# Kernel tuning notes

Measured on AMD Instinct MI355X. Metric: run time of the kernel, lower is better.

The kernel has to match this reference:

```python
import jax, jax.numpy as jnp
import numpy as np

BS, SL, FD = 8192, 49, 11
D_MODEL, DM2, HEAD = 128, 64, 8
NH, NHID, NLAYER = DM2 // HEAD, 4, 2
ABF = 1.0
XY_IDX = np.array([0, 1, 2, 3, 4, 5, 6, 7, 10])  # x feats + y feat (batch-normed cols)
DEC_IN = D_MODEL + 10  # d_model + len(x_dims + spa_dims)


def tanhshrink(x):
    return x - jnp.tanh(x)


def rope_angles(spa):
    # spa: [bs, sl, 2] -> per-token block angles [bs, sl, 4]
    # block order matches torch.block_diag(Rx(t0), Ry(t0), Rx(t1), Ry(t1))
    thetas = 10000.0 ** ((2.0 - 2.0 * jnp.arange(2, dtype=spa.dtype)) / 8.0)  # d=8, n_thetas=2
    ax = spa[..., 0:1] * thetas  # [bs, sl, 2]
    ay = spa[..., 1:2] * thetas
    return jnp.stack([ax[..., 0], ay[..., 0], ax[..., 1], ay[..., 1]], axis=-1)


def apply_rope(v, ang):
    # v: [bs, nh, s, 8]; ang: [bs, s, 4]. Applies the 8x8 block-diagonal
    # rotation directly on 2-d sub-pairs (same math as R @ v, no 8x8 matmats).
    c = jnp.cos(ang)[:, None]  # [bs, 1, s, 4]
    s = jnp.sin(ang)[:, None]
    v2 = v.reshape(*v.shape[:-1], 4, 2)
    r = jnp.stack([c * v2[..., 0] - s * v2[..., 1],
                   s * v2[..., 0] + c * v2[..., 1]], axis=-1)
    return r.reshape(v.shape)


def heads(x):  # [bs, s, dm2] -> [bs, nh, s, hd]
    b, s, _ = x.shape
    return x.reshape(b, s, NH, HEAD).transpose(0, 2, 1, 3)


def merge(x):  # [bs, nh, s, hd] -> [bs, s, dm2]
    b, h, s, d = x.shape
    return x.transpose(0, 2, 1, 3).reshape(b, s, h * d)


def mlp2(x, w1, b1, w2, b2):
    return tanhshrink(x @ w1 + b1) @ w2 + b2


def forward_impl(input_tensor, dists, bn_gamma, bn_beta,
                 xe_w1, xe_b1, xe_w2, xe_b2, ye_w1, ye_b1, ye_w2, ye_b2,
                 learnable_y, hidden_tokens, Wq, Wk, Wv, Wo, Wq2, Wk2, Wv2, Wo2,
                 dec_w0, dec_b0, dec_w1, dec_b1, dec_w2, dec_b2):
    bs = input_tensor.shape[0]
    # --- NanBatchNorm over x+y feature columns (no NaNs in clean inputs) ---
    xy = input_tensor[:, :, XY_IDX]
    mu = jnp.mean(xy, axis=(0, 1), keepdims=True)
    var = jnp.var(xy, axis=(0, 1), keepdims=True)
    xy = (xy - mu) / jnp.sqrt(var + 1e-5) * bn_gamma + bn_beta
    input_tensor = input_tensor.at[:, :, XY_IDX].set(xy)

    # --- target at last seq position: drop its dist, keep context dists ---
    dists_ctx = dists[:, :-1]                       # [bs, sl-1]
    central_x = input_tensor[:, -1:, :-1]           # [bs, 1, 10] (x + spa feats)

    # --- 2D RoPE angles from spatial coords ---
    ang = rope_angles(input_tensor[:, :, 8:10])     # [bs, sl, 4]

    # --- FCN encoders (two streams a=x, b=y) ---
    x_embed = mlp2(input_tensor[:, :, :8], xe_w1, xe_b1, xe_w2, xe_b2)      # [bs, sl, 64]
    y_embed = mlp2(input_tensor[:, :-1, 10:11], ye_w1, ye_b1, ye_w2, ye_b2)  # [bs, sl-1, 64]
    y_embed = jnp.concatenate([y_embed, jnp.broadcast_to(learnable_y, (bs, 1, DM2))], axis=1)

    ctx = (x_embed[:, :-1], y_embed[:, :-1])
    qry = (x_embed[:, -1:], y_embed[:, -1:])
    ang_ctx, ang_q = ang[:, :-1], ang[:, -1:]
    bias = (-ABF * dists_ctx)[:, None, None, :]     # [bs, 1, 1, sl-1]
    scale = 1.0 / jnp.sqrt(jnp.asarray(HEAD, input_tensor.dtype))

    outs, attn_ws = [], []
    for s in range(2):
        H = jnp.broadcast_to(hidden_tokens, (bs, NHID, DM2))
        for l in range(NLAYER):
            q = heads(H @ Wq[l, s])
            k = apply_rope(heads(ctx[s] @ Wk[l, s]), ang_ctx)
            v = heads(ctx[s] @ Wv[l, s])
            sc = jnp.einsum('bhqd,bhkd->bhqk', q, k) * scale + bias
            a = jax.nn.softmax(sc, axis=-1)
            H = H + merge(jnp.einsum('bhqk,bhkd->bhqd', a, v)) @ Wo[l, s]
        # query cross-attends the inducing tokens
        q = apply_rope(heads(qry[s] @ Wq2[s]), ang_q)
        k = heads(H @ Wk2[s])
        v = heads(H @ Wv2[s])
        sc = jnp.einsum('bhqd,bhkd->bhqk', q, k) * scale
        a = jax.nn.softmax(sc, axis=-1)
        outs.append(merge(jnp.einsum('bhqk,bhkd->bhqd', a, v)) @ Wo2[s])  # [bs, 1, 64]
        attn_ws.append(a)

    encoding = jnp.concatenate(outs, axis=-1)               # [bs, 1, 128]
    encoding = jnp.concatenate([encoding, central_x], axis=-1)  # [bs, 1, 138]
    h = tanhshrink(encoding @ dec_w0 + dec_b0)
    h = tanhshrink(h @ dec_w1 + dec_b1)
    pred = h @ dec_w2 + dec_b2                              # [bs, 1, 1]
    return pred


def setup_inputs() -> dict:
    key = jax.random.key(0)
    ks = jax.random.split(key, 32)
    g = lambda i, shape: 0.05 * jax.random.normal(ks[i], shape, dtype=jnp.float32)
    inp = {
        'input_tensor': jax.random.normal(ks[0], (BS, SL, FD), dtype=jnp.float32),
        'dists': jax.random.uniform(ks[1], (BS, SL), dtype=jnp.float32),
        'target_position': jnp.zeros((3, BS), dtype=jnp.int32),
        'bn_gamma': jnp.ones((9,), jnp.float32),
        'bn_beta': jnp.zeros((9,), jnp.float32),
        'xe_w1': g(2, (8, DM2)), 'xe_b1': jnp.zeros((DM2,), jnp.float32),
        'xe_w2': g(3, (DM2, DM2)), 'xe_b2': jnp.zeros((DM2,), jnp.float32),
        'ye_w1': g(4, (1, DM2)), 'ye_b1': jnp.zeros((DM2,), jnp.float32),
        'ye_w2': g(5, (DM2, DM2)), 'ye_b2': jnp.zeros((DM2,), jnp.float32),
        'learnable_y': g(6, (1, 1, DM2)),
        'hidden_tokens': g(7, (NHID, DM2)),
        'Wq': g(8, (NLAYER, 2, DM2, DM2)), 'Wk': g(9, (NLAYER, 2, DM2, DM2)),
        'Wv': g(10, (NLAYER, 2, DM2, DM2)), 'Wo': g(11, (NLAYER, 2, DM2, DM2)),
        'Wq2': g(12, (2, DM2, DM2)), 'Wk2': g(13, (2, DM2, DM2)),
        'Wv2': g(14, (2, DM2, DM2)), 'Wo2': g(15, (2, DM2, DM2)),
        'dec_w0': g(16, (DEC_IN, 512)), 'dec_b0': jnp.zeros((512,), jnp.float32),
        'dec_w1': g(17, (512, 256)), 'dec_b1': jnp.zeros((256,), jnp.float32),
        'dec_w2': g(18, (256, 1)), 'dec_b2': jnp.zeros((1,), jnp.float32),
    }
    return inp


def reference(input_tensor, dists, target_position, bn_gamma, bn_beta,
              xe_w1, xe_b1, xe_w2, xe_b2, ye_w1, ye_b1, ye_w2, ye_b2,
              learnable_y, hidden_tokens, Wq, Wk, Wv, Wo, Wq2, Wk2, Wv2, Wo2,
              dec_w0, dec_b0, dec_w1, dec_b1, dec_w2, dec_b2):
    # target_position is an index constant (query is the last token by construction)
    return forward_impl(input_tensor, dists, bn_gamma, bn_beta,
                        xe_w1, xe_b1, xe_w2, xe_b2, ye_w1, ye_b1, ye_w2, ye_b2,
                        learnable_y, hidden_tokens, Wq, Wk, Wv, Wo, Wq2, Wk2, Wv2, Wo2,
                        dec_w0, dec_b0, dec_w1, dec_b1, dec_w2, dec_b2)
```

## Files before the change

### kernel.cpp

```cpp
#include <hip/hip_runtime.h>
#include <math.h>

#define BS 8192
#define SL 49
#define FDIM 11
#define ROWS (BS*SL)

__device__ __forceinline__ float tanhshrink_f(float x) {
  float e = __expf(2.f * x);
  return (x - 1.f) + __fdividef(2.f, e + 1.f);
}

__global__ __launch_bounds__(256) void k_stats(const float* __restrict__ inp,
                                               double* __restrict__ gsum) {
  const int nblk = gridDim.x;
  const int per = (ROWS + nblk - 1) / nblk;
  const int r0 = blockIdx.x * per;
  int r1 = r0 + per; if (r1 > ROWS) r1 = ROWS;
  float s[9], q[9];
#pragma unroll
  for (int j = 0; j < 9; ++j) { s[j] = 0.f; q[j] = 0.f; }
  for (int r = r0 + threadIdx.x; r < r1; r += 256) {
    const float* row = inp + r * FDIM;
#pragma unroll
    for (int j = 0; j < 9; ++j) {
      float v = row[j < 8 ? j : 10];
      s[j] += v; q[j] += v * v;
    }
  }
#pragma unroll
  for (int j = 0; j < 9; ++j) {
    for (int off = 32; off; off >>= 1) {
      s[j] += __shfl_down(s[j], off);
      q[j] += __shfl_down(q[j], off);
    }
  }
  __shared__ float red[4][18];
  const int wid = threadIdx.x >> 6;
  const int lane = threadIdx.x & 63;
  if (lane == 0) {
#pragma unroll
    for (int j = 0; j < 9; ++j) { red[wid][j] = s[j]; red[wid][9 + j] = q[j]; }
  }
  __syncthreads();
  if (threadIdx.x < 18) {
    float t = red[0][threadIdx.x] + red[1][threadIdx.x] +
              red[2][threadIdx.x] + red[3][threadIdx.x];
    atomicAdd(&gsum[threadIdx.x], (double)t);
  }
}

__global__ __launch_bounds__(256) void k_finalize(const double* __restrict__ gsum,
                           const float* __restrict__ gamma,
                           const float* __restrict__ beta,
                           const float* __restrict__ hidden,
                           const float* __restrict__ Wq,
                           float* __restrict__ bnp,
                           float* __restrict__ q0g) {
  int tid = threadIdx.x;
  if (tid < 9) {
    const double N = (double)ROWS;
    double mean = gsum[tid] / N;
    double msq  = gsum[9 + tid] / N;
    float var = (float)(msq - mean * mean);
    float sc = gamma[tid] / sqrtf(var + 1e-5f);
    bnp[tid] = sc;
    bnp[9 + tid] = beta[tid] - (float)mean * sc;
  }
  int s = tid >> 7, i2 = (tid >> 6) & 1, c = tid & 63;
  const float* W = Wq + (s << 12);
#pragma unroll
  for (int ii = 0; ii < 2; ++ii) {
    int i = i2 + 2 * ii;
    float a = 0.f;
    for (int k = 0; k < 64; ++k) a += hidden[i * 64 + k] * W[k * 64 + c];
    q0g[s * 256 + i * 64 + c] = a;
  }
}

__global__ __launch_bounds__(256, 4) void k_mega(
    const float* __restrict__ inp, const float* __restrict__ dists,
    const float* __restrict__ bnp, const float* __restrict__ q0g,
    const float* __restrict__ xe_w1, const float* __restrict__ xe_b1,
    const float* __restrict__ xe_w2, const float* __restrict__ xe_b2,
    const float* __restrict__ ye_w1, const float* __restrict__ ye_b1,
    const float* __restrict__ ye_w2, const float* __restrict__ ye_b2,
    const float* __restrict__ learnable_y, const float* __restrict__ hidden_tokens,
    const float* __restrict__ Wq, const float* __restrict__ Wk,
    const float* __restrict__ Wv, const float* __restrict__ Wo,
    const float* __restrict__ Wq2, const float* __restrict__ Wk2,
    const float* __restrict__ Wv2, const float* __restrict__ Wo2,
    float* __restrict__ enc)
{
  __shared__ float raw[49][12];
  __shared__ float cs8[49][8];
  __shared__ float emb[49][64];
  __shared__ float KB[49][68];
  __shared__ float scb[32][52];
  __shared__ float Hs[4][64];
  __shared__ float qb[4][64];
  __shared__ float db[48];
  __shared__ float bnl[18];
  __shared__ float q2[64];
  __shared__ float o1[64];
  __shared__ float a2[32];

  const int tid  = threadIdx.x;
  const int lane = tid & 63;
  const int grp  = tid >> 6;
  const int b    = blockIdx.x >> 1;
  const int s    = blockIdx.x & 1;
  const float scale = 0.35355339059327373f;

  for (int i = tid; i < 49 * FDIM; i += 256) raw[i / FDIM][i % FDIM] = inp[b * (49*FDIM) + i];
  if (tid < 18) bnl[tid] = bnp[tid];
  if (tid >= 64 && tid < 112) db[tid - 64] = dists[b * 49 + (tid - 64)];
  __syncthreads();

  if (tid < 49) {
    float x = raw[tid][8], y = raw[tid][9];
    cs8[tid][0] = cosf(10.f * x); cs8[tid][1] = cosf(10.f * y);
    cs8[tid][2] = cosf(x);        cs8[tid][3] = cosf(y);
    cs8[tid][4] = sinf(10.f * x); cs8[tid][5] = sinf(10.f * y);
    cs8[tid][6] = sinf(x);        cs8[tid][7] = sinf(y);
  }
  for (int i = tid; i < 441; i += 256) {
    int t = i / 9, j = i - t * 9;
    int f = (j < 8) ? j : 10;
    raw[t][f] = raw[t][f] * bnl[j] + bnl[9 + j];
  }
  __syncthreads();

  if (s == 0 && tid < 10) enc[b * 138 + 128 + tid] = raw[48][tid];

  if (s == 0) {
    const float bias1 = xe_b1[lane];
    float acc[13];
#pragma unroll
    for (int j = 0; j < 13; ++j) acc[j] = bias1;
#pragma unroll
    for (int k = 0; k < 8; ++k) {
      float w = xe_w1[k * 64 + lane];
#pragma unroll
      for (int j = 0; j < 13; ++j) {
        int t = grp + 4 * j;
        if (t < 49) acc[j] += raw[t][k] * w;
      }
    }
#pragma unroll
    for (int j = 0; j < 13; ++j) {
      int t = grp + 4 * j;
      if (t < 49) KB[t][lane] = tanhshrink_f(acc[j]);
    }
  } else {
    const float w1y = ye_w1[lane];
    const float b1y = ye_b1[lane];
#pragma unroll
    for (int j = 0; j < 12; ++j) {
      int t = grp + 4 * j;
      KB[t][lane] = tanhshrink_f(raw[t][10] * w1y + b1y);
    }
  }
  __syncthreads();

  if (s == 0) {
    const float b2 = xe_b2[lane];
    float acc[13];
#pragma unroll
    for (int j = 0; j < 13; ++j) acc[j] = b2;
    for (int k = 0; k < 64; k += 4) {
      float w0 = xe_w2[(k + 0) * 64 + lane];
      float w1_ = xe_w2[(k + 1) * 64 + lane];
      float w2_ = xe_w2[(k + 2) * 64 + lane];
      float w3_ = xe_w2[(k + 3) * 64 + lane];
#pragma unroll
      for (int j = 0; j < 13; ++j) {
        int t = grp + 4 * j;
        if (t < 49) {
          float4 cv = *(const float4*)&KB[t][k];
          acc[j] += cv.x * w0 + cv.y * w1_ + cv.z * w2_ + cv.w * w3_;
        }
      }
    }
#pragma unroll
    for (int j = 0; j < 13; ++j) {
      int t = grp + 4 * j;
      if (t < 49) emb[t][lane] = acc[j];
    }
  } else {
    const float b2 = ye_b2[lane];
    float acc[12];
#pragma unroll
    for (int j = 0; j < 12; ++j) acc[j] = b2;
    for (int k = 0; k < 64; k += 4) {
      float w0 = ye_w2[(k + 0) * 64 + lane];
      float w1_ = ye_w2[(k + 1) * 64 + lane];
      float w2_ = ye_w2[(k + 2) * 64 + lane];
      float w3_ = ye_w2[(k + 3) * 64 + lane];
#pragma unroll
      for (int j = 0; j < 12; ++j) {
        float4 cv = *(const float4*)&KB[grp + 4 * j][k];
        acc[j] += cv.x * w0 + cv.y * w1_ + cv.z * w2_ + cv.w * w3_;
      }
    }
#pragma unroll
    for (int j = 0; j < 12; ++j) emb[grp + 4 * j][lane] = acc[j];
    if (tid < 64) emb[48][lane] = learnable_y[lane];
  }
  Hs[grp][lane] = hidden_tokens[grp * 64 + lane];
  __syncthreads();

#pragma unroll 1
  for (int l = 0; l < 2; ++l) {
    const float* Wk_p = Wk + ((l * 2 + s) << 12);
    const float* Wv_p = Wv + ((l * 2 + s) << 12);
    const float* Wo_p = Wo + ((l * 2 + s) << 12);
    if (l == 0) {
      qb[grp][lane] = q0g[s * 256 + tid];
    } else {
      const float* Wq_p = Wq + ((l * 2 + s) << 12);
      float a = 0.f;
      for (int k = 0; k < 64; k += 4) {
        float4 hv = *(const float4*)&Hs[grp][k];
        a += hv.x * Wq_p[(k + 0) * 64 + lane] + hv.y * Wq_p[(k + 1) * 64 + lane]
           + hv.z * Wq_p[(k + 2) * 64 + lane] + hv.w * Wq_p[(k + 3) * 64 + lane];
      }
      qb[grp][lane] = a;
    }
    {
      float aK[12];
#pragma unroll
      for (int j = 0; j < 12; ++j) aK[j] = 0.f;
      for (int k = 0; k < 64; k += 4) {
        float wk0 = Wk_p[(k + 0) * 64 + lane], wk1 = Wk_p[(k + 1) * 64 + lane];
        float wk2 = Wk_p[(k + 2) * 64 + lane], wk3 = Wk_p[(k + 3) * 64 + lane];
#pragma unroll
        for (int j = 0; j < 12; ++j) {
          float4 cv = *(const float4*)&emb[grp + 4 * j][k];
          aK[j] += cv.x * wk0 + cv.y * wk1 + cv.z * wk2 + cv.w * wk3;
        }
      }
      const int p = (lane >> 1) & 3;
      const int odd = lane & 1;
#pragma unroll
      for (int j = 0; j < 12; ++j) {
        int t = grp + 4 * j;
        float other = __shfl_xor(aK[j], 1);
        float co = cs8[t][p], si = cs8[t][4 + p];
        KB[t][lane] = odd ? (si * other + co * aK[j]) : (co * aK[j] - si * other);
      }
    }
    __syncthreads();
    {
      const int t0 = tid & 7;
      const int i  = (tid >> 3) & 3;
      const int h  = tid >> 5;
      const int r  = tid >> 3;
      float4 qa = *(const float4*)&qb[i][h * 8];
      float4 qc = *(const float4*)&qb[i][h * 8 + 4];
      float v[6];
#pragma unroll
      for (int j = 0; j < 6; ++j) {
        int t = t0 + 8 * j;
        float4 ka = *(const float4*)&KB[t][h * 8];
        float4 kc = *(const float4*)&KB[t][h * 8 + 4];
        float a = qa.x * ka.x + qa.y * ka.y + qa.z * ka.z + qa.w * ka.w
                + qc.x * kc.x + qc.y * kc.y + qc.z * kc.z + qc.w * kc.w;
        v[j] = a * scale - db[t];
      }
      float m = fmaxf(fmaxf(fmaxf(v[0], v[1]), fmaxf(v[2], v[3])), fmaxf(v[4], v[5]));
      m = fmaxf(m, __shfl_xor(m, 1));
      m = fmaxf(m, __shfl_xor(m, 2));
      m = fmaxf(m, __shfl_xor(m, 4));
      float sum = 0.f;
#pragma unroll
      for (int j = 0; j < 6; ++j) { v[j] = __expf(v[j] - m); sum += v[j]; }
      sum += __shfl_xor(sum, 1);
      sum += __shfl_xor(sum, 2);
      sum += __shfl_xor(sum, 4);
      float inv = 1.f / sum;
#pragma unroll
      for (int j = 0; j < 6; ++j) scb[r][t0 + 8 * j] = v[j] * inv;
    }
    __syncthreads();
    {
      float acc[8];
#pragma unroll
      for (int m = 0; m < 8; ++m) acc[m] = 0.f;
      for (int tt = 0; tt < 48; tt += 4) {
        float e0 = emb[tt + 0][lane], e1 = emb[tt + 1][lane];
        float e2 = emb[tt + 2][lane], e3 = emb[tt + 3][lane];
#pragma unroll
        for (int m = 0; m < 8; ++m) {
          float4 sc4 = *(const float4*)&scb[grp + 4 * m][tt];
          acc[m] += sc4.x * e0 + sc4.y * e1 + sc4.z * e2 + sc4.w * e3;
        }
      }
#pragma unroll
      for (int m = 0; m < 8; ++m) KB[grp + 4 * m][lane] = acc[m];
    }
    __syncthreads();
    {
      const int r = ((lane >> 3) << 2) + grp;
      float a = 0.f;
      for (int c = 0; c < 64; c += 4) {
        float4 tv = *(const float4*)&KB[r][c];
        a += tv.x * Wv_p[(c + 0) * 64 + lane] + tv.y * Wv_p[(c + 1) * 64 + lane]
           + tv.z * Wv_p[(c + 2) * 64 + lane] + tv.w * Wv_p[(c + 3) * 64 + lane];
      }
      qb[grp][lane] = a;
    }
    __syncthreads();
    {
      float a = Hs[grp][lane];
      for (int k = 0; k < 64; k += 4) {
        float4 av = *(const float4*)&qb[grp][k];
        a += av.x * Wo_p[(k + 0) * 64 + lane] + av.y * Wo_p[(k + 1) * 64 + lane]
           + av.z * Wo_p[(k + 2) * 64 + lane] + av.w * Wo_p[(k + 3) * 64 + lane];
      }
      Hs[grp][lane] = a;
    }
    __syncthreads();
  }

  const float* Wq2_p = Wq2 + (s << 12);
  const float* Wk2_p = Wk2 + (s << 12);
  const float* Wv2_p = Wv2 + (s << 12);
  const float* Wo2_p = Wo2 + (s << 12);
  if (tid < 64) {
    float a = 0.f;
    for (int k = 0; k < 64; k += 4) {
      float4 cv = *(const float4*)&emb[48][k];
      a += cv.x * Wq2_p[(k + 0) * 64 + lane] + cv.y * Wq2_p[(k + 1) * 64 + lane]
         + cv.z * Wq2_p[(k + 2) * 64 + lane] + cv.w * Wq2_p[(k + 3) * 64 + lane];
    }
    float other = __shfl_xor(a, 1);
    int p = (lane >> 1) & 3;
    float co = cs8[48][p], si = cs8[48][4 + p];
    q2[lane] = (lane & 1) ? (si * other + co * a) : (co * a - si * other);
  }
  {
    float aK = 0.f, aV = 0.f;
    for (int k = 0; k < 64; k += 4) {
      float4 hv = *(const float4*)&Hs[grp][k];
      aK += hv.x * Wk2_p[(k + 0) * 64 + lane] + hv.y * Wk2_p[(k + 1) * 64 + lane]
          + hv.z * Wk2_p[(k + 2) * 64 + lane] + hv.w * Wk2_p[(k + 3) * 64 + lane];
      aV += hv.x * Wv2_p[(k + 0) * 64 + lane] + hv.y * Wv2_p[(k + 1) * 64 + lane]
          + hv.z * Wv2_p[(k + 2) * 64 + lane] + hv.w * Wv2_p[(k + 3) * 64 + lane];
    }
    KB[grp][lane] = aK;
    KB[8 + grp][lane] = aV;
  }
  __syncthreads();
  if (tid < 32) {
    int h = tid >> 2, i = tid & 3;
    float a = 0.f;
#pragma unroll
    for (int d = 0; d < 8; ++d) a += q2[h * 8 + d] * KB[i][h * 8 + d];
    a *= scale;
    float m = fmaxf(a, __shfl_xor(a, 1));
    m = fmaxf(m, __shfl_xor(m, 2));
    float e = __expf(a - m);
    float sum = e + __shfl_xor(e, 1);
    sum += __shfl_xor(sum, 2);
    a2[tid] = e / sum;
  }
  __syncthreads();
  if (tid < 64) {
    int h = lane >> 3;
    float a = 0.f;
#pragma unroll
    for (int i = 0; i < 4; ++i) a += a2[h * 4 + i] * KB[8 + i][lane];
    o1[lane] = a;
  }
  __syncthreads();
  if (tid < 64) {
    float a = 0.f;
    for (int k = 0; k < 64; k += 4) {
      float4 ov = *(const float4*)&o1[k];
      a += ov.x * Wo2_p[(k + 0) * 64 + lane] + ov.y * Wo2_p[(k + 1) * 64 + lane]
         + ov.z * Wo2_p[(k + 2) * 64 + lane] + ov.w * Wo2_p[(k + 3) * 64 + lane];
    }
    enc[b * 138 + s * 64 + lane] = a;
  }
}

__global__ __launch_bounds__(256) void k_dec(
    const float* __restrict__ enc,
    const float* __restrict__ w0, const float* __restrict__ b0,
    const float* __restrict__ w1, const float* __restrict__ b1,
    const float* __restrict__ w2, const float* __restrict__ b2,
    float* __restrict__ out)
{
  __shared__ float encs[16][140];
  __shared__ float h0s[16][512];
  __shared__ float h1s[16][256];
  const int tid = threadIdx.x;
  const int rb = blockIdx.x * 16;

  for (int i = tid; i < 16 * 138; i += 256) {
    int r = i / 138, k = i - r * 138;
    encs[r][k] = enc[(rb + r) * 138 + k];
  }
  __syncthreads();
  {
    float acc0[16], acc1[16];
    const float bb0 = b0[tid], bb1 = b0[tid + 256];
#pragma unroll
    for (int r = 0; r < 16; ++r) { acc0[r] = bb0; acc1[r] = bb1; }
    for (int k = 0; k < 136; k += 4) {
      float wa0 = w0[(k + 0) * 512 + tid], wa1 = w0[(k + 1) * 512 + tid];
      float wa2 = w0[(k + 2) * 512 + tid], wa3 = w0[(k + 3) * 512 + tid];
      float wb0 = w0[(k + 0) * 512 + tid + 256], wb1 = w0[(k + 1) * 512 + tid + 256];
      float wb2 = w0[(k + 2) * 512 + tid + 256], wb3 = w0[(k + 3) * 512 + tid + 256];
#pragma unroll
      for (int r = 0; r < 16; ++r) {
        float4 ev = *(const float4*)&encs[r][k];
        acc0[r] += ev.x * wa0 + ev.y * wa1 + ev.z * wa2 + ev.w * wa3;
        acc1[r] += ev.x * wb0 + ev.y * wb1 + ev.z * wb2 + ev.w * wb3;
      }
    }
    for (int k = 136; k < 138; ++k) {
      float wa = w0[k * 512 + tid], wb = w0[k * 512 + tid + 256];
#pragma unroll
      for (int r = 0; r < 16; ++r) {
        float e = encs[r][k];
        acc0[r] += e * wa; acc1[r] += e * wb;
      }
    }
#pragma unroll
    for (int r = 0; r < 16; ++r) {
      float a = acc0[r]; h0s[r][tid] = a - tanhf(a);
      a = acc1[r];       h0s[r][tid + 256] = a - tanhf(a);
    }
  }
  __syncthreads();
  {
    float acc[16];
    const float bb = b1[tid];
#pragma unroll
    for (int r = 0; r < 16; ++r) acc[r] = bb;
    for (int k = 0; k < 512; k += 4) {
      float ww0 = w1[(k + 0) * 256 + tid], ww1 = w1[(k + 1) * 256 + tid];
      float ww2 = w1[(k + 2) * 256 + tid], ww3 = w1[(k + 3) * 256 + tid];
#pragma unroll
      for (int r = 0; r < 16; ++r) {
        float4 hv = *(const float4*)&h0s[r][k];
        acc[r] += hv.x * ww0 + hv.y * ww1 + hv.z * ww2 + hv.w * ww3;
      }
    }
#pragma unroll
    for (int r = 0; r < 16; ++r) { float a = acc[r]; h1s[r][tid] = a - tanhf(a); }
  }
  __syncthreads();
  {
    int r = tid >> 4, l16 = tid & 15;
    float a = 0.f;
    for (int kk = 0; kk < 16; ++kk) {
      int k = l16 + 16 * kk;
      a += h1s[r][k] * w2[k];
    }
    for (int off = 8; off; off >>= 1) a += __shfl_down(a, off, 16);
    if (l16 == 0) out[rb + r] = a + b2[0];
  }
}

extern "C" void kernel_launch(void* const* d_in, const int* in_sizes, int n_in,
                              void* d_out, int out_size, void* d_ws, size_t ws_size,
                              hipStream_t stream) {
  const float* inp        = (const float*)d_in[0];
  const float* dists      = (const float*)d_in[1];
  const float* bn_gamma   = (const float*)d_in[3];
  const float* bn_beta    = (const float*)d_in[4];
  const float* xe_w1      = (const float*)d_in[5];
  const float* xe_b1      = (const float*)d_in[6];
  const float* xe_w2      = (const float*)d_in[7];
  const float* xe_b2      = (const float*)d_in[8];
  const float* ye_w1      = (const float*)d_in[9];
  const float* ye_b1      = (const float*)d_in[10];
  const float* ye_w2      = (const float*)d_in[11];
  const float* ye_b2      = (const float*)d_in[12];
  const float* learnable  = (const float*)d_in[13];
  const float* hidden     = (const float*)d_in[14];
  const float* Wq         = (const float*)d_in[15];
  const float* Wk         = (const float*)d_in[16];
  const float* Wv         = (const float*)d_in[17];
  const float* Wo         = (const float*)d_in[18];
  const float* Wq2        = (const float*)d_in[19];
  const float* Wk2        = (const float*)d_in[20];
  const float* Wv2        = (const float*)d_in[21];
  const float* Wo2        = (const float*)d_in[22];
  const float* dec_w0     = (const float*)d_in[23];
  const float* dec_b0     = (const float*)d_in[24];
  const float* dec_w1     = (const float*)d_in[25];
  const float* dec_b1     = (const float*)d_in[26];
  const float* dec_w2     = (const float*)d_in[27];
  const float* dec_b2     = (const float*)d_in[28];

  double* gsum = (double*)d_ws;
  float*  bnp  = (float*)((char*)d_ws + 256);
  float*  q0g  = (float*)((char*)d_ws + 512);
  float*  enc  = (float*)((char*)d_ws + 2560);

  hipMemsetAsync(d_ws, 0, 256, stream);
  k_stats   <<<512, 256, 0, stream>>>(inp, gsum);
  k_finalize<<<1, 256, 0, stream>>>(gsum, bn_gamma, bn_beta, hidden, Wq, bnp, q0g);
  k_mega    <<<BS * 2, 256, 0, stream>>>(inp, dists, bnp, q0g,
                                         xe_w1, xe_b1, xe_w2, xe_b2,
                                         ye_w1, ye_b1, ye_w2, ye_b2,
                                         learnable, hidden,
                                         Wq, Wk, Wv, Wo, Wq2, Wk2, Wv2, Wo2, enc);
  k_dec     <<<BS / 16, 256, 0, stream>>>(enc, dec_w0, dec_b0, dec_w1, dec_b1,
                                          dec_w2, dec_b2, (float*)d_out);
}
```

Measured before the change: 1.009 ms.

## Use split-bf16 MFMA for embedding second layer and K projections

Replaces the FP32 FMA loops for the encoder second MLP layer and the per-layer K projections with 16x16x32 bf16 MFMA instructions. Both operands are split into high and low bf16 halves (three MFMAs per step), which keeps close to fp32 accuracy. A new prep kernel pre-splits and transposes the weights each call. Shared memory is repacked with aliased buffers and XOR-swizzled bf16 tiles, the last token's embedding is computed separately, and launch bounds drop to 3 waves per SIMD. It trades extra MFMA work and conversion overhead for fewer VALU cycles, at some risk of small precision drift.

```diff
diff --git a/kernel.cpp b/kernel.cpp
--- a/kernel.cpp
+++ b/kernel.cpp
@@ -6,6 +6,17 @@
 #define FDIM 11
 #define ROWS (BS*SL)
 
+typedef __attribute__((ext_vector_type(8))) short bf16x8;
+typedef __attribute__((ext_vector_type(4))) float f32x4;
+
+__device__ __forceinline__ unsigned short f2bf(float f) {
+  unsigned u = __float_as_uint(f);
+  u += 0x7FFFu + ((u >> 16) & 1u);
+  return (unsigned short)(u >> 16);
+}
+__device__ __forceinline__ float bf2f(unsigned short h) {
+  return __uint_as_float(((unsigned)h) << 16);
+}
 __device__ __forceinline__ float tanhshrink_f(float x) {
   float e = __expf(2.f * x);
   return (x - 1.f) + __fdividef(2.f, e + 1.f);
@@ -78,47 +89,76 @@
   }
 }
 
-__global__ __launch_bounds__(256, 4) void k_mega(
+__global__ __launch_bounds__(256) void k_prep(const float* __restrict__ xe_w2,
+                                              const float* __restrict__ ye_w2,
+                                              const float* __restrict__ Wk,
+                                              unsigned short* __restrict__ wb) {
+  int idx = blockIdx.x * 256 + threadIdx.x;
+  int mat = idx >> 12;
+  int e = idx & 4095;
+  int n = e >> 6, k = e & 63;
+  float v; unsigned short *dh, *dl;
+  if (mat == 0)      { v = xe_w2[k * 64 + n]; dh = wb;          dl = wb + 4096;  }
+  else if (mat == 1) { v = ye_w2[k * 64 + n]; dh = wb + 8192;   dl = wb + 12288; }
+  else { int m = mat - 2; v = Wk[(m << 12) + k * 64 + n];
+         dh = wb + 16384 + (m << 12); dl = wb + 32768 + (m << 12); }
+  unsigned short h = f2bf(v);
+  dh[e] = h;
+  dl[e] = f2bf(v - bf2f(h));
+}
+
+__global__ __launch_bounds__(256, 3) void k_mega(
     const float* __restrict__ inp, const float* __restrict__ dists,
     const float* __restrict__ bnp, const float* __restrict__ q0g,
+    const unsigned short* __restrict__ wb,
     const float* __restrict__ xe_w1, const float* __restrict__ xe_b1,
     const float* __restrict__ xe_w2, const float* __restrict__ xe_b2,
     const float* __restrict__ ye_w1, const float* __restrict__ ye_b1,
-    const float* __restrict__ ye_w2, const float* __restrict__ ye_b2,
+    const float* __restrict__ ye_b2,
     const float* __restrict__ learnable_y, const float* __restrict__ hidden_tokens,
-    const float* __restrict__ Wq, const float* __restrict__ Wk,
+    const float* __restrict__ Wq,
     const float* __restrict__ Wv, const float* __restrict__ Wo,
     const float* __restrict__ Wq2, const float* __restrict__ Wk2,
     const float* __restrict__ Wv2, const float* __restrict__ Wo2,
     float* __restrict__ enc)
 {
-  __shared__ float raw[49][12];
-  __shared__ float cs8[49][8];
-  __shared__ float emb[49][64];
-  __shared__ float KB[49][68];
-  __shared__ float scb[32][52];
-  __shared__ float Hs[4][64];
-  __shared__ float qb[4][64];
-  __shared__ float db[48];
-  __shared__ float bnl[18];
-  __shared__ float q2[64];
-  __shared__ float o1[64];
-  __shared__ float a2[32];
+  __shared__ __align__(16) float KBf[48 * 68];
+  __shared__ __align__(16) unsigned short AstBuf[2 * 48 * 72];
+  __shared__ __align__(16) float embf[48 * 64];
+  __shared__ __align__(16) unsigned short EMBh[48 * 64];
+  __shared__ __align__(16) unsigned short EMBl[48 * 64];
+  __shared__ __align__(16) float cs8[49][8];
+  __shared__ __align__(16) float Hs[4 * 64];
+
+  float* rawp = KBf;
+  float* h1q  = KBf + 588;
+  float* bnlp = KBf + 652;
+  unsigned short* Asth = AstBuf;
+  unsigned short* Astl = AstBuf + 48 * 72;
+  float* fbuf = (float*)AstBuf;
+  float* scb  = fbuf;
+  float* qbf  = fbuf + 1664;
+  float* dbp  = fbuf + 1920;
+  float* embq = fbuf + 1968;
+  float* q2   = fbuf + 2032;
+  float* o1   = fbuf + 2096;
+  float* a2   = fbuf + 2160;
 
   const int tid  = threadIdx.x;
   const int lane = tid & 63;
   const int grp  = tid >> 6;
+  const int l15  = lane & 15;
+  const int quad = lane >> 4;
   const int b    = blockIdx.x >> 1;
   const int s    = blockIdx.x & 1;
   const float scale = 0.35355339059327373f;
 
-  for (int i = tid; i < 49 * FDIM; i += 256) raw[i / FDIM][i % FDIM] = inp[b * (49*FDIM) + i];
-  if (tid < 18) bnl[tid] = bnp[tid];
-  if (tid >= 64 && tid < 112) db[tid - 64] = dists[b * 49 + (tid - 64)];
+  for (int i = tid; i < 49 * FDIM; i += 256) rawp[(i / FDIM) * 12 + (i % FDIM)] = inp[b * (49 * FDIM) + i];
+  if (tid < 18) bnlp[tid] = bnp[tid];
   __syncthreads();
 
   if (tid < 49) {
-    float x = raw[tid][8], y = raw[tid][9];
+    float x = rawp[tid * 12 + 8], y = rawp[tid * 12 + 9];
     cs8[tid][0] = cosf(10.f * x); cs8[tid][1] = cosf(10.f * y);
     cs8[tid][2] = cosf(x);        cs8[tid][3] = cosf(y);
     cs8[tid][4] = sinf(10.f * x); cs8[tid][5] = sinf(10.f * y);
@@ -127,127 +167,144 @@
   for (int i = tid; i < 441; i += 256) {
     int t = i / 9, j = i - t * 9;
     int f = (j < 8) ? j : 10;
-    raw[t][f] = raw[t][f] * bnl[j] + bnl[9 + j];
-  }
-  __syncthreads();
-
-  if (s == 0 && tid < 10) enc[b * 138 + 128 + tid] = raw[48][tid];
+    rawp[t * 12 + f] = rawp[t * 12 + f] * bnlp[j] + bnlp[9 + j];
+  }
+  __syncthreads();
+
+  if (s == 0 && tid < 10) enc[b * 138 + 128 + tid] = rawp[48 * 12 + tid];
 
   if (s == 0) {
     const float bias1 = xe_b1[lane];
-    float acc[13];
-#pragma unroll
-    for (int j = 0; j < 13; ++j) acc[j] = bias1;
+    float acc[12];
+    float acc12 = bias1;
+#pragma unroll
+    for (int j = 0; j < 12; ++j) acc[j] = bias1;
 #pragma unroll
     for (int k = 0; k < 8; ++k) {
       float w = xe_w1[k * 64 + lane];
 #pragma unroll
-      for (int j = 0; j < 13; ++j) {
-        int t = grp + 4 * j;
-        if (t < 49) acc[j] += raw[t][k] * w;
-      }
-    }
-#pragma unroll
-    for (int j = 0; j < 13; ++j) {
+      for (int j = 0; j < 12; ++j) acc[j] += rawp[(grp + 4 * j) * 12 + k] * w;
+      acc12 += rawp[48 * 12 + k] * w;
+    }
+#pragma unroll
+    for (int j = 0; j < 12; ++j) {
       int t = grp + 4 * j;
-      if (t < 49) KB[t][lane] = tanhshrink_f(acc[j]);
-    }
+      float a = tanhshrink_f(acc[j]);
+      unsigned short h = f2bf(a);
+      Asth[t * 72 + lane] = h;
+      Astl[t * 72 + lane] = f2bf(a - bf2f(h));
+    }
+    if (grp == 0) h1q[lane] = tanhshrink_f(acc12);
   } else {
     const float w1y = ye_w1[lane];
     const float b1y = ye_b1[lane];
 #pragma unroll
     for (int j = 0; j < 12; ++j) {
       int t = grp + 4 * j;
-      KB[t][lane] = tanhshrink_f(raw[t][10] * w1y + b1y);
-    }
-  }
-  __syncthreads();
-
-  if (s == 0) {
-    const float b2 = xe_b2[lane];
-    float acc[13];
-#pragma unroll
-    for (int j = 0; j < 13; ++j) acc[j] = b2;
-    for (int k = 0; k < 64; k += 4) {
-      float w0 = xe_w2[(k + 0) * 64 + lane];
-      float w1_ = xe_w2[(k + 1) * 64 + lane];
-      float w2_ = xe_w2[(k + 2) * 64 + lane];
-      float w3_ = xe_w2[(k + 3) * 64 + lane];
-#pragma unroll
-      for (int j = 0; j < 13; ++j) {
-        int t = grp + 4 * j;
-        if (t < 49) {
-          float4 cv = *(const float4*)&KB[t][k];
-          acc[j] += cv.x * w0 + cv.y * w1_ + cv.z * w2_ + cv.w * w3_;
-        }
-      }
-    }
-#pragma unroll
-    for (int j = 0; j < 13; ++j) {
-      int t = grp + 4 * j;
-      if (t < 49) emb[t][lane] = acc[j];
-    }
-  } else {
-    const float b2 = ye_b2[lane];
-    float acc[12];
-#pragma unroll
-    for (int j = 0; j < 12; ++j) acc[j] = b2;
-    for (int k = 0; k < 64; k += 4) {
-      float w0 = ye_w2[(k + 0) * 64 + lane];
-      float w1_ = ye_w2[(k + 1) * 64 + lane];
-      float w2_ = ye_w2[(k + 2) * 64 + lane];
-      float w3_ = ye_w2[(k + 3) * 64 + lane];
-#pragma unroll
-      for (int j = 0; j < 12; ++j) {
-        float4 cv = *(const float4*)&KB[grp + 4 * j][k];
-        acc[j] += cv.x * w0 + cv.y * w1_ + cv.z * w2_ + cv.w * w3_;
-      }
-    }
-#pragma unroll
-    for (int j = 0; j < 12; ++j) emb[grp + 4 * j][lane] = acc[j];
-    if (tid < 64) emb[48][lane] = learnable_y[lane];
-  }
-  Hs[grp][lane] = hidden_tokens[grp * 64 + lane];
+      float a = tanhshrink_f(rawp[t * 12 + 10] * w1y + b1y);
+      unsigned short h = f2bf(a);
+      Asth[t * 72 + lane] = h;
+      Astl[t * 72 + lane] = f2bf(a - bf2f(h));
+    }
+  }
+  __syncthreads();
+
+  {
+    const unsigned short* BTh = s ? (wb + 8192)  : wb;
+    const unsigned short* BTl = s ? (wb + 12288) : (wb + 4096);
+    const float* b2p = s ? ye_b2 : xe_b2;
+#pragma unroll 1
+    for (int i = 0; i < 3; ++i) {
+      int T = grp + 4 * i;
+      int rt = T % 3, ct = T / 3;
+      int arow = rt * 16 + l15;
+      int bcol = ct * 16 + l15;
+      f32x4 acc = {0.f, 0.f, 0.f, 0.f};
+#pragma unroll
+      for (int ks = 0; ks < 2; ++ks) {
+        int ko = ks * 32 + quad * 8;
+        bf16x8 Ah = *(bf16x8*)&Asth[arow * 72 + ko];
+        bf16x8 Al = *(bf16x8*)&Astl[arow * 72 + ko];
+        bf16x8 Bh = *(const bf16x8*)(BTh + bcol * 64 + ko);
+        bf16x8 Bl = *(const bf16x8*)(BTl + bcol * 64 + ko);
+        acc = __builtin_amdgcn_mfma_f32_16x16x32_bf16(Ah, Bh, acc, 0, 0, 0);
+        acc = __builtin_amdgcn_mfma_f32_16x16x32_bf16(Al, Bh, acc, 0, 0, 0);
+        acc = __builtin_amdgcn_mfma_f32_16x16x32_bf16(Ah, Bl, acc, 0, 0, 0);
+      }
+      float bias = b2p[bcol];
+#pragma unroll
+      for (int r = 0; r < 4; ++r) {
+        int t = rt * 16 + quad * 4 + r;
+        float v = acc[r] + bias;
+        embf[t * 64 + bcol] = v;
+        int sw = (t & 3) << 4;
+        unsigned short h = f2bf(v);
+        EMBh[t * 64 + (bcol ^ sw)] = h;
+        EMBl[t * 64 + (bcol ^ sw)] = f2bf(v - bf2f(h));
+      }
+    }
+  }
+  float r48 = 0.f;
+  if (s == 0 && tid < 64) {
+    r48 = xe_b2[lane];
+    for (int k = 0; k < 64; ++k) r48 += h1q[k] * xe_w2[k * 64 + lane];
+  }
+  __syncthreads();
+
+  if (tid < 64) embq[lane] = (s == 0) ? r48 : learnable_y[lane];
+  if (tid >= 64 && tid < 112) dbp[tid - 64] = dists[b * 49 + (tid - 64)];
+  Hs[grp * 64 + lane] = hidden_tokens[grp * 64 + lane];
   __syncthreads();
 
 #pragma unroll 1
   for (int l = 0; l < 2; ++l) {
-    const float* Wk_p = Wk + ((l * 2 + s) << 12);
     const float* Wv_p = Wv + ((l * 2 + s) << 12);
     const float* Wo_p = Wo + ((l * 2 + s) << 12);
     if (l == 0) {
-      qb[grp][lane] = q0g[s * 256 + tid];
+      qbf[tid] = q0g[s * 256 + tid];
     } else {
-      const float* Wq_p = Wq + ((l * 2 + s) << 12);
+      const float* Wq_p = Wq + ((2 + s) << 12);
       float a = 0.f;
       for (int k = 0; k < 64; k += 4) {
-        float4 hv = *(const float4*)&Hs[grp][k];
+        float4 hv = *(float4*)&Hs[grp * 64 + k];
         a += hv.x * Wq_p[(k + 0) * 64 + lane] + hv.y * Wq_p[(k + 1) * 64 + lane]
            + hv.z * Wq_p[(k + 2) * 64 + lane] + hv.w * Wq_p[(k + 3) * 64 + lane];
       }
-      qb[grp][lane] = a;
+      qbf[tid] = a;
     }
     {
-      float aK[12];
-#pragma unroll
-      for (int j = 0; j < 12; ++j) aK[j] = 0.f;
-      for (int k = 0; k < 64; k += 4) {
-        float wk0 = Wk_p[(k + 0) * 64 + lane], wk1 = Wk_p[(k + 1) * 64 + lane];
-        float wk2 = Wk_p[(k + 2) * 64 + lane], wk3 = Wk_p[(k + 3) * 64 + lane];
-#pragma unroll
-        for (int j = 0; j < 12; ++j) {
-          float4 cv = *(const float4*)&emb[grp + 4 * j][k];
-          aK[j] += cv.x * wk0 + cv.y * wk1 + cv.z * wk2 + cv.w * wk3;
-        }
-      }
-      const int p = (lane >> 1) & 3;
-      const int odd = lane & 1;
-#pragma unroll
-      for (int j = 0; j < 12; ++j) {
-        int t = grp + 4 * j;
-        float other = __shfl_xor(aK[j], 1);
-        float co = cs8[t][p], si = cs8[t][4 + p];
-        KB[t][lane] = odd ? (si * other + co * aK[j]) : (co * aK[j] - si * other);
+      const unsigned short* ATh = wb + 16384 + ((l * 2 + s) << 12);
+      const unsigned short* ATl = wb + 32768 + ((l * 2 + s) << 12);
+      const int arow = grp * 16 + l15;
+      bf16x8 Ah0 = *(const bf16x8*)(ATh + arow * 64 + quad * 8);
+      bf16x8 Ah1 = *(const bf16x8*)(ATh + arow * 64 + 32 + quad * 8);
+      bf16x8 Al0 = *(const bf16x8*)(ATl + arow * 64 + quad * 8);
+      bf16x8 Al1 = *(const bf16x8*)(ATl + arow * 64 + 32 + quad * 8);
+      const int p0 = (quad * 2) & 3, p1 = (quad * 2 + 1) & 3;
+      const int c0 = grp * 16 + quad * 4;
+#pragma unroll 1
+      for (int nt = 0; nt < 3; ++nt) {
+        const int tcol = nt * 16 + l15;
+        const int sw = (tcol & 3) << 4;
+        int k0 = (quad * 8) ^ sw;
+        int k1 = (32 + quad * 8) ^ sw;
+        bf16x8 Bh0 = *(bf16x8*)&EMBh[tcol * 64 + k0];
+        bf16x8 Bl0 = *(bf16x8*)&EMBl[tcol * 64 + k0];
+        bf16x8 Bh1 = *(bf16x8*)&EMBh[tcol * 64 + k1];
+        bf16x8 Bl1 = *(bf16x8*)&EMBl[tcol * 64 + k1];
+        f32x4 acc = {0.f, 0.f, 0.f, 0.f};
+        acc = __builtin_amdgcn_mfma_f32_16x16x32_bf16(Ah0, Bh0, acc, 0, 0, 0);
+        acc = __builtin_amdgcn_mfma_f32_16x16x32_bf16(Al0, Bh0, acc, 0, 0, 0);
+        acc = __builtin_amdgcn_mfma_f32_16x16x32_bf16(Ah0, Bl0, acc, 0, 0, 0);
+        acc = __builtin_amdgcn_mfma_f32_16x16x32_bf16(Ah1, Bh1, acc, 0, 0, 0);
+        acc = __builtin_amdgcn_mfma_f32_16x16x32_bf16(Al1, Bh1, acc, 0, 0, 0);
+        acc = __builtin_amdgcn_mfma_f32_16x16x32_bf16(Ah1, Bl1, acc, 0, 0, 0);
+        float co0 = cs8[tcol][p0], si0 = cs8[tcol][4 + p0];
+        float co1 = cs8[tcol][p1], si1 = cs8[tcol][4 + p1];
+        KBf[tcol * 68 + c0 + 0] = co0 * acc[0] - si0 * acc[1];
+        KBf[tcol * 68 + c0 + 1] = si0 * acc[0] + co0 * acc[1];
+        KBf[tcol * 68 + c0 + 2] = co1 * acc[2] - si1 * acc[3];
+        KBf[tcol * 68 + c0 + 3] = si1 * acc[2] + co1 * acc[3];
       }
     }
     __syncthreads();
@@ -256,17 +313,17 @@
       const int i  = (tid >> 3) & 3;
       const int h  = tid >> 5;
       const int r  = tid >> 3;
-      float4 qa = *(const float4*)&qb[i][h * 8];
-      float4 qc = *(const float4*)&qb[i][h * 8 + 4];
+      float4 qa = *(float4*)&qbf[i * 64 + h * 8];
+      float4 qc = *(float4*)&qbf[i * 64 + h * 8 + 4];
       float v[6];
 #pragma unroll
       for (int j = 0; j < 6; ++j) {
         int t = t0 + 8 * j;
-        float4 ka = *(const float4*)&KB[t][h * 8];
-        float4 kc = *(const float4*)&KB[t][h * 8 + 4];
+        float4 ka = *(float4*)&KBf[t * 68 + h * 8];
+        float4 kc = *(float4*)&KBf[t * 68 + h * 8 + 4];
         float a = qa.x * ka.x + qa.y * ka.y + qa.z * ka.z + qa.w * ka.w
                 + qc.x * kc.x + qc.y * kc.y + qc.z * kc.z + qc.w * kc.w;
-        v[j] = a * scale - db[t];
+        v[j] = a * scale - dbp[t];
       }
       float m = fmaxf(fmaxf(fmaxf(v[0], v[1]), fmaxf(v[2], v[3])), fmaxf(v[4], v[5]));
       m = fmaxf(m, __shfl_xor(m, 1));
@@ -280,7 +337,7 @@
       sum += __shfl_xor(sum, 4);
       float inv = 1.f / sum;
 #pragma unroll
-      for (int j = 0; j < 6; ++j) scb[r][t0 + 8 * j] = v[j] * inv;
+      for (int j = 0; j < 6; ++j) scb[r * 52 + t0 + 8 * j] = v[j] * inv;
     }
     __syncthreads();
     {
@@ -288,37 +345,37 @@
 #pragma unroll
       for (int m = 0; m < 8; ++m) acc[m] = 0.f;
       for (int tt = 0; tt < 48; tt += 4) {
-        float e0 = emb[tt + 0][lane], e1 = emb[tt + 1][lane];
-        float e2 = emb[tt + 2][lane], e3 = emb[tt + 3][lane];
+        float e0 = embf[(tt + 0) * 64 + lane], e1 = embf[(tt + 1) * 64 + lane];
+        float e2 = embf[(tt + 2) * 64 + lane], e3 = embf[(tt + 3) * 64 + lane];
 #pragma unroll
         for (int m = 0; m < 8; ++m) {
-          float4 sc4 = *(const float4*)&scb[grp + 4 * m][tt];
+          float4 sc4 = *(float4*)&scb[(grp + 4 * m) * 52 + tt];
           acc[m] += sc4.x * e0 + sc4.y * e1 + sc4.z * e2 + sc4.w * e3;
         }
       }
 #pragma unroll
-      for (int m = 0; m < 8; ++m) KB[grp + 4 * m][lane] = acc[m];
+      for (int m = 0; m < 8; ++m) KBf[(grp + 4 * m) * 68 + lane] = acc[m];
     }
     __syncthreads();
     {
       const int r = ((lane >> 3) << 2) + grp;
       float a = 0.f;
       for (int c = 0; c < 64; c += 4) {
-        float4 tv = *(const float4*)&KB[r][c];
+        float4 tv = *(float4*)&KBf[r * 68 + c];
         a += tv.x * Wv_p[(c + 0) * 64 + lane] + tv.y * Wv_p[(c + 1) * 64 + lane]
            + tv.z * Wv_p[(c + 2) * 64 + lane] + tv.w * Wv_p[(c + 3) * 64 + lane];
       }
-      qb[grp][lane] = a;
+      qbf[tid] = a;
     }
     __syncthreads();
     {
-      float a = Hs[grp][lane];
+      float a = Hs[grp * 64 + lane];
       for (int k = 0; k < 64; k += 4) {
-        float4 av = *(const float4*)&qb[grp][k];
+        float4 av = *(float4*)&qbf[grp * 64 + k];
         a += av.x * Wo_p[(k + 0) * 64 + lane] + av.y * Wo_p[(k + 1) * 64 + lane]
            + av.z * Wo_p[(k + 2) * 64 + lane] + av.w * Wo_p[(k + 3) * 64 + lane];
       }
-      Hs[grp][lane] = a;
+      Hs[grp * 64 + lane] = a;
     }
     __syncthreads();
   }
@@ -330,7 +387,7 @@
   if (tid < 64) {
     float a = 0.f;
     for (int k = 0; k < 64; k += 4) {
-      float4 cv = *(const float4*)&emb[48][k];
+      float4 cv = *(float4*)&embq[k];
       a += cv.x * Wq2_p[(k + 0) * 64 + lane] + cv.y * Wq2_p[(k + 1) * 64 + lane]
          + cv.z * Wq2_p[(k + 2) * 64 + lane] + cv.w * Wq2_p[(k + 3) * 64 + lane];
     }
@@ -342,21 +399,21 @@
   {
     float aK = 0.f, aV = 0.f;
     for (int k = 0; k < 64; k += 4) {
-      float4 hv = *(const float4*)&Hs[grp][k];
+      float4 hv = *(float4*)&Hs[grp * 64 + k];
       aK += hv.x * Wk2_p[(k + 0) * 64 + lane] + hv.y * Wk2_p[(k + 1) * 64 + lane]
           + hv.z * Wk2_p[(k + 2) * 64 + lane] + hv.w * Wk2_p[(k + 3) * 64 + lane];
       aV += hv.x * Wv2_p[(k + 0) * 64 + lane] + hv.y * Wv2_p[(k + 1) * 64 + lane]
           + hv.z * Wv2_p[(k + 2) * 64 + lane] + hv.w * Wv2_p[(k + 3) * 64 + lane];
     }
-    KB[grp][lane] = aK;
-    KB[8 + grp][lane] = aV;
+    KBf[grp * 68 + lane] = aK;
+    KBf[(8 + grp) * 68 + lane] = aV;
   }
   __syncthreads();
   if (tid < 32) {
     int h = tid >> 2, i = tid & 3;
     float a = 0.f;
 #pragma unroll
-    for (int d = 0; d < 8; ++d) a += q2[h * 8 + d] * KB[i][h * 8 + d];
+    for (int d = 0; d < 8; ++d) a += q2[h * 8 + d] * KBf[i * 68 + h * 8 + d];
     a *= scale;
     float m = fmaxf(a, __shfl_xor(a, 1));
     m = fmaxf(m, __shfl_xor(m, 2));
@@ -370,14 +427,14 @@
     int h = lane >> 3;
     float a = 0.f;
 #pragma unroll
-    for (int i = 0; i < 4; ++i) a += a2[h * 4 + i] * KB[8 + i][lane];
+    for (int i = 0; i < 4; ++i) a += a2[h * 4 + i] * KBf[(8 + i) * 68 + lane];
     o1[lane] = a;
   }
   __syncthreads();
   if (tid < 64) {
     float a = 0.f;
     for (int k = 0; k < 64; k += 4) {
-      float4 ov = *(const float4*)&o1[k];
+      float4 ov = *(float4*)&o1[k];
       a += ov.x * Wo2_p[(k + 0) * 64 + lane] + ov.y * Wo2_p[(k + 1) * 64 + lane]
          + ov.z * Wo2_p[(k + 2) * 64 + lane] + ov.w * Wo2_p[(k + 3) * 64 + lane];
     }
@@ -421,11 +478,11 @@
       }
     }
     for (int k = 136; k < 138; ++k) {
-      float wa = w0[k * 512 + tid], wb = w0[k * 512 + tid + 256];
+      float wa = w0[k * 512 + tid], wbv = w0[k * 512 + tid + 256];
 #pragma unroll
       for (int r = 0; r < 16; ++r) {
         float e = encs[r][k];
-        acc0[r] += e * wa; acc1[r] += e * wb;
+        acc0[r] += e * wa; acc1[r] += e * wbv;
       }
     }
 #pragma unroll
@@ -501,15 +558,17 @@
   float*  bnp  = (float*)((char*)d_ws + 256);
   float*  q0g  = (float*)((char*)d_ws + 512);
   float*  enc  = (float*)((char*)d_ws + 2560);
+  unsigned short* wbuf = (unsigned short*)((char*)d_ws + 4524544);
 
   hipMemsetAsync(d_ws, 0, 256, stream);
   k_stats   <<<512, 256, 0, stream>>>(inp, gsum);
   k_finalize<<<1, 256, 0, stream>>>(gsum, bn_gamma, bn_beta, hidden, Wq, bnp, q0g);
-  k_mega    <<<BS * 2, 256, 0, stream>>>(inp, dists, bnp, q0g,
+  k_prep    <<<96, 256, 0, stream>>>(xe_w2, ye_w2, Wk, wbuf);
+  k_mega    <<<BS * 2, 256, 0, stream>>>(inp, dists, bnp, q0g, wbuf,
                                          xe_w1, xe_b1, xe_w2, xe_b2,
-                                         ye_w1, ye_b1, ye_w2, ye_b2,
+                                         ye_w1, ye_b1, ye_b2,
                                          learnable, hidden,
-                                         Wq, Wk, Wv, Wo, Wq2, Wk2, Wv2, Wo2, enc);
+                                         Wq, Wv, Wo, Wq2, Wk2, Wv2, Wo2, enc);
   k_dec     <<<BS / 16, 256, 0, stream>>>(enc, dec_w0, dec_b0, dec_w1, dec_b1,
                                           dec_w2, dec_b2, (float*)d_out);
 }
```

New measurement: 1.424 ms. 1.41x slower.

## Remap encoder threads to 32-row groups with two output columns each

Applied to the files above, without the earlier changes.

Changes the thread-to-output mapping in the per-sample encoder kernel. Each thread now handles two feature columns across six rows instead of one column across twelve rows, in the embedding MLPs, the K projection with rope, and the attention-weighted sum. Each shared-memory row read now feeds two accumulators and each weight load is spread over fewer rows, which cuts LDS traffic per FMA. It also drops the branch-divergent t<49 guards by handling row 48 separately, at the cost of a serial 64-iteration loop on one warp-slice for that row.

```diff
diff --git a/kernel.cpp b/kernel.cpp
--- a/kernel.cpp
+++ b/kernel.cpp
@@ -108,6 +108,8 @@
   const int tid  = threadIdx.x;
   const int lane = tid & 63;
   const int grp  = tid >> 6;
+  const int rg   = tid >> 5;
+  const int cg   = tid & 31;
   const int b    = blockIdx.x >> 1;
   const int s    = blockIdx.x & 1;
   const float scale = 0.35355339059327373f;
@@ -134,78 +136,86 @@
   if (s == 0 && tid < 10) enc[b * 138 + 128 + tid] = raw[48][tid];
 
   if (s == 0) {
-    const float bias1 = xe_b1[lane];
-    float acc[13];
-#pragma unroll
-    for (int j = 0; j < 13; ++j) acc[j] = bias1;
-#pragma unroll
-    for (int k = 0; k < 8; ++k) {
-      float w = xe_w1[k * 64 + lane];
-#pragma unroll
-      for (int j = 0; j < 13; ++j) {
-        int t = grp + 4 * j;
-        if (t < 49) acc[j] += raw[t][k] * w;
-      }
-    }
-#pragma unroll
-    for (int j = 0; j < 13; ++j) {
-      int t = grp + 4 * j;
-      if (t < 49) KB[t][lane] = tanhshrink_f(acc[j]);
+    float wA[8], wB[8];
+#pragma unroll
+    for (int k = 0; k < 8; ++k) { wA[k] = xe_w1[k * 64 + cg]; wB[k] = xe_w1[k * 64 + cg + 32]; }
+    const float bA = xe_b1[cg], bB = xe_b1[cg + 32];
+#pragma unroll
+    for (int m = 0; m < 6; ++m) {
+      int t = rg + 8 * m;
+      float4 r0 = *(const float4*)&raw[t][0];
+      float4 r1 = *(const float4*)&raw[t][4];
+      float a = bA + r0.x*wA[0] + r0.y*wA[1] + r0.z*wA[2] + r0.w*wA[3]
+                   + r1.x*wA[4] + r1.y*wA[5] + r1.z*wA[6] + r1.w*wA[7];
+      float c = bB + r0.x*wB[0] + r0.y*wB[1] + r0.z*wB[2] + r0.w*wB[3]
+                   + r1.x*wB[4] + r1.y*wB[5] + r1.z*wB[6] + r1.w*wB[7];
+      KB[t][cg]      = tanhshrink_f(a);
+      KB[t][cg + 32] = tanhshrink_f(c);
+    }
+    if (rg == 0) {
+      float4 r0 = *(const float4*)&raw[48][0];
+      float4 r1 = *(const float4*)&raw[48][4];
+      float a = bA + r0.x*wA[0] + r0.y*wA[1] + r0.z*wA[2] + r0.w*wA[3]
+                   + r1.x*wA[4] + r1.y*wA[5] + r1.z*wA[6] + r1.w*wA[7];
+      float c = bB + r0.x*wB[0] + r0.y*wB[1] + r0.z*wB[2] + r0.w*wB[3]
+                   + r1.x*wB[4] + r1.y*wB[5] + r1.z*wB[6] + r1.w*wB[7];
+      KB[48][cg]      = tanhshrink_f(a);
+      KB[48][cg + 32] = tanhshrink_f(c);
     }
   } else {
-    const float w1y = ye_w1[lane];
-    const float b1y = ye_b1[lane];
-#pragma unroll
-    for (int j = 0; j < 12; ++j) {
-      int t = grp + 4 * j;
-      KB[t][lane] = tanhshrink_f(raw[t][10] * w1y + b1y);
-    }
-  }
-  __syncthreads();
-
-  if (s == 0) {
-    const float b2 = xe_b2[lane];
-    float acc[13];
-#pragma unroll
-    for (int j = 0; j < 13; ++j) acc[j] = b2;
+    const float wA = ye_w1[cg], wB = ye_w1[cg + 32];
+    const float bA = ye_b1[cg], bB = ye_b1[cg + 32];
+#pragma unroll
+    for (int m = 0; m < 6; ++m) {
+      int t = rg + 8 * m;
+      float x = raw[t][10];
+      KB[t][cg]      = tanhshrink_f(x * wA + bA);
+      KB[t][cg + 32] = tanhshrink_f(x * wB + bB);
+    }
+  }
+  __syncthreads();
+
+  {
+    const float* W2  = s ? ye_w2 : xe_w2;
+    const float* b2p = s ? ye_b2 : xe_b2;
+    float accA[6], accB[6];
+    const float bA = b2p[cg], bB = b2p[cg + 32];
+#pragma unroll
+    for (int m = 0; m < 6; ++m) { accA[m] = bA; accB[m] = bB; }
     for (int k = 0; k < 64; k += 4) {
-      float w0 = xe_w2[(k + 0) * 64 + lane];
-      float w1_ = xe_w2[(k + 1) * 64 + lane];
-      float w2_ = xe_w2[(k + 2) * 64 + lane];
-      float w3_ = xe_w2[(k + 3) * 64 + lane];
-#pragma unroll
-      for (int j = 0; j < 13; ++j) {
-        int t = grp + 4 * j;
-        if (t < 49) {
-          float4 cv = *(const float4*)&KB[t][k];
-          acc[j] += cv.x * w0 + cv.y * w1_ + cv.z * w2_ + cv.w * w3_;
+      float wA0 = W2[(k + 0) * 64 + cg],      wA1 = W2[(k + 1) * 64 + cg];
+      float wA2 = W2[(k + 2) * 64 + cg],      wA3 = W2[(k + 3) * 64 + cg];
+      float wB0 = W2[(k + 0) * 64 + cg + 32], wB1 = W2[(k + 1) * 64 + cg + 32];
+      float wB2 = W2[(k + 2) * 64 + cg + 32], wB3 = W2[(k + 3) * 64 + cg + 32];
+#pragma unroll
+      for (int m = 0; m < 6; ++m) {
+        float4 a = *(const float4*)&KB[rg + 8 * m][k];
+        accA[m] += a.x * wA0 + a.y * wA1 + a.z * wA2 + a.w * wA3;
+        accB[m] += a.x * wB0 + a.y * wB1 + a.z * wB2 + a.w * wB3;
+      }
+    }
+#pragma unroll
+    for (int m = 0; m < 6; ++m) {
+      int t = rg + 8 * m;
+      emb[t][cg]      = accA[m];
+      emb[t][cg + 32] = accB[m];
+    }
+    if (s == 0) {
+      if (rg == 0) {
+        float a = bA, c = bB;
+        for (int k = 0; k < 64; k += 4) {
+          float4 h4 = *(const float4*)&KB[48][k];
+          a += h4.x * W2[(k+0)*64+cg]      + h4.y * W2[(k+1)*64+cg]
+             + h4.z * W2[(k+2)*64+cg]      + h4.w * W2[(k+3)*64+cg];
+          c += h4.x * W2[(k+0)*64+cg+32]   + h4.y * W2[(k+1)*64+cg+32]
+             + h4.z * W2[(k+2)*64+cg+32]   + h4.w * W2[(k+3)*64+cg+32];
         }
-      }
-    }
-#pragma unroll
-    for (int j = 0; j < 13; ++j) {
-      int t = grp + 4 * j;
-      if (t < 49) emb[t][lane] = acc[j];
-    }
-  } else {
-    const float b2 = ye_b2[lane];
-    float acc[12];
-#pragma unroll
-    for (int j = 0; j < 12; ++j) acc[j] = b2;
-    for (int k = 0; k < 64; k += 4) {
-      float w0 = ye_w2[(k + 0) * 64 + lane];
-      float w1_ = ye_w2[(k + 1) * 64 + lane];
-      float w2_ = ye_w2[(k + 2) * 64 + lane];
-      float w3_ = ye_w2[(k + 3) * 64 + lane];
-#pragma unroll
-      for (int j = 0; j < 12; ++j) {
-        float4 cv = *(const float4*)&KB[grp + 4 * j][k];
-        acc[j] += cv.x * w0 + cv.y * w1_ + cv.z * w2_ + cv.w * w3_;
-      }
-    }
-#pragma unroll
-    for (int j = 0; j < 12; ++j) emb[grp + 4 * j][lane] = acc[j];
-    if (tid < 64) emb[48][lane] = learnable_y[lane];
+        emb[48][cg]      = a;
+        emb[48][cg + 32] = c;
+      }
+    } else {
+      if (tid < 64) emb[48][lane] = learnable_y[lane];
+    }
   }
   Hs[grp][lane] = hidden_tokens[grp * 64 + lane];
   __syncthreads();
@@ -218,7 +228,7 @@
     if (l == 0) {
       qb[grp][lane] = q0g[s * 256 + tid];
     } else {
-      const float* Wq_p = Wq + ((l * 2 + s) << 12);
+      const float* Wq_p = Wq + ((2 + s) << 12);
       float a = 0.f;
       for (int k = 0; k < 64; k += 4) {
         float4 hv = *(const float4*)&Hs[grp][k];
@@ -228,26 +238,31 @@
       qb[grp][lane] = a;
     }
     {
-      float aK[12];
-#pragma unroll
-      for (int j = 0; j < 12; ++j) aK[j] = 0.f;
+      float aK0[6], aK1[6];
+#pragma unroll
+      for (int m = 0; m < 6; ++m) { aK0[m] = 0.f; aK1[m] = 0.f; }
       for (int k = 0; k < 64; k += 4) {
-        float wk0 = Wk_p[(k + 0) * 64 + lane], wk1 = Wk_p[(k + 1) * 64 + lane];
-        float wk2 = Wk_p[(k + 2) * 64 + lane], wk3 = Wk_p[(k + 3) * 64 + lane];
-#pragma unroll
-        for (int j = 0; j < 12; ++j) {
-          float4 cv = *(const float4*)&emb[grp + 4 * j][k];
-          aK[j] += cv.x * wk0 + cv.y * wk1 + cv.z * wk2 + cv.w * wk3;
+        float wA0 = Wk_p[(k + 0) * 64 + cg],      wA1 = Wk_p[(k + 1) * 64 + cg];
+        float wA2 = Wk_p[(k + 2) * 64 + cg],      wA3 = Wk_p[(k + 3) * 64 + cg];
+        float wB0 = Wk_p[(k + 0) * 64 + cg + 32], wB1 = Wk_p[(k + 1) * 64 + cg + 32];
+        float wB2 = Wk_p[(k + 2) * 64 + cg + 32], wB3 = Wk_p[(k + 3) * 64 + cg + 32];
+#pragma unroll
+        for (int m = 0; m < 6; ++m) {
+          float4 a = *(const float4*)&emb[rg + 8 * m][k];
+          aK0[m] += a.x * wA0 + a.y * wA1 + a.z * wA2 + a.w * wA3;
+          aK1[m] += a.x * wB0 + a.y * wB1 + a.z * wB2 + a.w * wB3;
         }
       }
-      const int p = (lane >> 1) & 3;
-      const int odd = lane & 1;
-#pragma unroll
-      for (int j = 0; j < 12; ++j) {
-        int t = grp + 4 * j;
-        float other = __shfl_xor(aK[j], 1);
+      const int p = (cg >> 1) & 3;
+      const int odd = cg & 1;
+#pragma unroll
+      for (int m = 0; m < 6; ++m) {
+        int t = rg + 8 * m;
+        float o0 = __shfl_xor(aK0[m], 1);
+        float o1v = __shfl_xor(aK1[m], 1);
         float co = cs8[t][p], si = cs8[t][4 + p];
-        KB[t][lane] = odd ? (si * other + co * aK[j]) : (co * aK[j] - si * other);
+        KB[t][cg]      = odd ? (si * o0 + co * aK0[m]) : (co * aK0[m] - si * o0);
+        KB[t][cg + 32] = odd ? (si * o1v + co * aK1[m]) : (co * aK1[m] - si * o1v);
       }
     }
     __syncthreads();
@@ -284,20 +299,26 @@
     }
     __syncthreads();
     {
-      float acc[8];
-#pragma unroll
-      for (int m = 0; m < 8; ++m) acc[m] = 0.f;
+      float accA[4], accB[4];
+#pragma unroll
+      for (int m = 0; m < 4; ++m) { accA[m] = 0.f; accB[m] = 0.f; }
       for (int tt = 0; tt < 48; tt += 4) {
-        float e0 = emb[tt + 0][lane], e1 = emb[tt + 1][lane];
-        float e2 = emb[tt + 2][lane], e3 = emb[tt + 3][lane];
-#pragma unroll
-        for (int m = 0; m < 8; ++m) {
-          float4 sc4 = *(const float4*)&scb[grp + 4 * m][tt];
-          acc[m] += sc4.x * e0 + sc4.y * e1 + sc4.z * e2 + sc4.w * e3;
+        float2 e0 = *(const float2*)&emb[tt + 0][2 * cg];
+        float2 e1 = *(const float2*)&emb[tt + 1][2 * cg];
+        float2 e2 = *(const float2*)&emb[tt + 2][2 * cg];
+        float2 e3 = *(const float2*)&emb[tt + 3][2 * cg];
+#pragma unroll
+        for (int m = 0; m < 4; ++m) {
+          float4 sc4 = *(const float4*)&scb[rg + 8 * m][tt];
+          accA[m] += sc4.x * e0.x + sc4.y * e1.x + sc4.z * e2.x + sc4.w * e3.x;
+          accB[m] += sc4.x * e0.y + sc4.y * e1.y + sc4.z * e2.y + sc4.w * e3.y;
         }
       }
 #pragma unroll
-      for (int m = 0; m < 8; ++m) KB[grp + 4 * m][lane] = acc[m];
+      for (int m = 0; m < 4; ++m) {
+        float2 w2v; w2v.x = accA[m]; w2v.y = accB[m];
+        *(float2*)&KB[rg + 8 * m][2 * cg] = w2v;
+      }
     }
     __syncthreads();
     {
@@ -421,11 +442,11 @@
       }
     }
     for (int k = 136; k < 138; ++k) {
-      float wa = w0[k * 512 + tid], wb = w0[k * 512 + tid + 256];
+      float wa = w0[k * 512 + tid], wbv = w0[k * 512 + tid + 256];
 #pragma unroll
       for (int r = 0; r < 16; ++r) {
         float e = encs[r][k];
-        acc0[r] += e * wa; acc1[r] += e * wb;
+        acc0[r] += e * wa; acc1[r] += e * wbv;
       }
     }
 #pragma unroll
```

Result: slower. 1.469 ms (+45.6%).
